# Performance work log

Measured on AMD Instinct MI355X. Metric: run time of the kernel, lower is better.

The kernel has to match this reference:

```python
import jax, jax.numpy as jnp
import numpy as np

D_MODEL = 1024
NUM_EXPERTS = 8


def setup_inputs() -> dict:
    key = jax.random.key(0)
    k_x, k_wg, k_bg, k_we, k_be = jax.random.split(key, 5)
    B, S, D, E = 4, 2048, D_MODEL, NUM_EXPERTS
    x = jax.random.normal(k_x, (B, S, D), dtype=jnp.float32)
    # gate: nn.Linear(d_model, num_experts) -> weight [E, D], bias [E]
    Wg = jax.random.normal(k_wg, (E, D), dtype=jnp.float32) * 0.02
    bg = jax.random.normal(k_bg, (E,), dtype=jnp.float32) * 0.02
    # experts: E x nn.Linear(d_model, d_model) -> weights [E, D, D], biases [E, D]
    We = jax.random.normal(k_we, (E, D, D), dtype=jnp.float32) * 0.02
    be = jax.random.normal(k_be, (E, D), dtype=jnp.float32) * 0.02
    return {"x": x, "Wg": Wg, "bg": bg, "We": We, "be": be, "top_k": 2}


def reference(x, Wg, bg, We, be, top_k):
    # gate_scores: softmax over experts. x:[B,S,D], Wg:[E,D] -> [B,S,E]
    gate_scores = jax.nn.softmax(jnp.einsum("bsd,ed->bse", x, Wg) + bg, axis=-1)
    top_k_values, top_k_indices = jax.lax.top_k(gate_scores, top_k)  # [B,S,K]
    # dense all-expert compute (faithful to original): [B,S,D,E]
    expert_outputs = jnp.einsum("bsd,ekd->bske", x, We) + be.T  # be.T: [D,E]
    # gather top-k experts along last dim: idx broadcast over feature dim D
    top_k_outputs = jnp.take_along_axis(
        expert_outputs, top_k_indices[:, :, None, :], axis=-1
    )  # [B,S,D,K]
    weighted = (top_k_outputs * top_k_values[:, :, None, :]).sum(axis=-1)  # [B,S,D]
    return weighted
```

## Files before the change

### kernel.cpp

```cpp
#include <hip/hip_runtime.h>
#include <hip/hip_bf16.h>
#include <stdint.h>

#define D_MODEL 1024
#define NUM_EXPERTS 8
#define NBUCKET 16
#define BM 128
#define BN 128
#define BK 64
#define KSTEPS (D_MODEL / BK)
#define GATE_TOK 16
#define GATE_BLOCKS 512
#define CONV_BLOCKS 4096
#define GEMM_GRID 2048
#define NWORK 8192

typedef __bf16 bf16x8 __attribute__((ext_vector_type(8)));
typedef float f32x4 __attribute__((ext_vector_type(4)));
typedef unsigned short u16x8 __attribute__((ext_vector_type(8)));

__device__ __forceinline__ unsigned short f32_to_bf16_rne(float f) {
    union { float f; uint32_t u; } v;
    v.f = f;
    uint32_t u = v.u;
    u += 0x7FFFu + ((u >> 16) & 1u);
    return (unsigned short)(u >> 16);
}

__device__ __forceinline__ float bf16_to_f32(unsigned short h) {
    union { uint32_t u; float f; } v;
    v.u = ((uint32_t)h) << 16;
    return v.f;
}

__device__ __forceinline__ void gload_lds16(const unsigned short* g, unsigned short* l) {
    __builtin_amdgcn_global_load_lds(
        (const __attribute__((address_space(1))) void*)g,
        (__attribute__((address_space(3))) void*)l,
        16, 0, 0);
}

__global__ __launch_bounds__(256) void prep_kernel(
    const float* __restrict__ x, const float* __restrict__ Wg,
    const float* __restrict__ bg, const float* __restrict__ We, int T,
    int* __restrict__ counts, int* __restrict__ token_list,
    float* __restrict__ gate_list, unsigned short* __restrict__ xb,
    unsigned short* __restrict__ wbv)
{
    const int tid = threadIdx.x;

    if (blockIdx.x >= GATE_BLOCKS) {
        int g = (blockIdx.x - GATE_BLOCKS) * 256 + tid;
        int s   = g & 7;
        int kt  = (g >> 3) & (KSTEPS - 1);
        int n   = (g >> 7) & 1023;
        int e   = g >> 17;

        const float* sp = We + (size_t)g * 8;
        float4 a = ((const float4*)sp)[0];
        float4 b = ((const float4*)sp)[1];
        u16x8 o;
        o[0] = f32_to_bf16_rne(a.x);
        o[1] = f32_to_bf16_rne(a.y);
        o[2] = f32_to_bf16_rne(a.z);
        o[3] = f32_to_bf16_rne(a.w);
        o[4] = f32_to_bf16_rne(b.x);
        o[5] = f32_to_bf16_rne(b.y);
        o[6] = f32_to_bf16_rne(b.z);
        o[7] = f32_to_bf16_rne(b.w);

        int ss = s ^ (n & 7);
        unsigned short* dp =
            wbv + (((size_t)(e * KSTEPS + kt) * 1024 + n) * BK) + ss * 8;
        *(u16x8*)dp = o;
        return;
    }

    const int lane = tid & 63;
    const int wave = tid >> 6;
    const int tokBase = blockIdx.x * GATE_TOK;

    __shared__ float4 WgS[NUM_EXPERTS * 256];
    __shared__ double logitS[GATE_TOK][NUM_EXPERTS];
    __shared__ int cntS[NBUCKET];
    __shared__ int baseS[NBUCKET];

    if (tid < NBUCKET) cntS[tid] = 0;
#pragma unroll
    for (int i = 0; i < 8; i++)
        WgS[i * 256 + tid] = ((const float4*)Wg)[i * 256 + tid];
    __syncthreads();

    for (int tt = 0; tt < GATE_TOK / 4; tt++) {
        const int lt = wave * (GATE_TOK / 4) + tt;
        const int token = tokBase + lt;
        const float4* xr4 = (const float4*)(x + (size_t)token * D_MODEL);
        ushort4* xbr4 = (ushort4*)(xb + (size_t)token * D_MODEL);

        float4 xv[4];
#pragma unroll
        for (int q = 0; q < 4; q++) {
            float4 f = xr4[q * 64 + lane];
            xv[q] = f;
            ushort4 o;
            o.x = f32_to_bf16_rne(f.x);
            o.y = f32_to_bf16_rne(f.y);
            o.z = f32_to_bf16_rne(f.z);
            o.w = f32_to_bf16_rne(f.w);
            xbr4[q * 64 + lane] = o;
        }

        double acc[NUM_EXPERTS];
#pragma unroll
        for (int e = 0; e < NUM_EXPERTS; e++) {
            double a = 0.0;
#pragma unroll
            for (int q = 0; q < 4; q++) {
                float4 w = WgS[e * 256 + q * 64 + lane];
                a += (double)xv[q].x * (double)w.x;
                a += (double)xv[q].y * (double)w.y;
                a += (double)xv[q].z * (double)w.z;
                a += (double)xv[q].w * (double)w.w;
            }
            acc[e] = a;
        }
#pragma unroll
        for (int e = 0; e < NUM_EXPERTS; e++) {
            double a = acc[e];
            for (int off = 32; off > 0; off >>= 1) a += __shfl_xor(a, off, 64);
            acc[e] = a;
        }
        if (lane == 0) {
#pragma unroll
            for (int e = 0; e < NUM_EXPERTS; e++)
                logitS[lt][e] = acc[e] + (double)bg[e];
        }
    }
    __syncthreads();

    int i1 = 0, i2 = 0, o1 = 0, o2 = 0;
    double v1d = 0.0, v2d = 0.0;
    const int token2 = tokBase + tid;
    if (tid < GATE_TOK) {
        double lg[NUM_EXPERTS];
#pragma unroll
        for (int e = 0; e < NUM_EXPERTS; e++) lg[e] = logitS[tid][e];
        i1 = 0;
#pragma unroll
        for (int e = 1; e < NUM_EXPERTS; e++) if (lg[e] > lg[i1]) i1 = e;
        i2 = (i1 == 0) ? 1 : 0;
#pragma unroll
        for (int e = 0; e < NUM_EXPERTS; e++)
            if (e != i1 && lg[e] > lg[i2]) i2 = e;
        double m = lg[i1], den = 0.0;
#pragma unroll
        for (int e = 0; e < NUM_EXPERTS; e++) den += exp(lg[e] - m);
        v1d = exp(lg[i1] - m) / den;
        v2d = exp(lg[i2] - m) / den;
        o1 = atomicAdd(&cntS[i1], 1);
        o2 = atomicAdd(&cntS[8 + i2], 1);
    }
    __syncthreads();
    if (tid < NBUCKET) baseS[tid] = atomicAdd(&counts[tid], cntS[tid]);
    __syncthreads();
    if (tid < GATE_TOK) {
        int p1 = i1 * T + baseS[i1] + o1;
        token_list[p1] = token2;
        gate_list[p1]  = (float)v1d;
        int p2 = (8 + i2) * T + baseS[8 + i2] + o2;
        token_list[p2] = token2;
        gate_list[p2]  = (float)v2d;
    }
}

__global__ __launch_bounds__(256) void moe_gemm(
    const unsigned short* __restrict__ xb,
    const unsigned short* __restrict__ wb,
    const float* __restrict__ be,
    const int* __restrict__ counts,
    const int* __restrict__ token_list,
    const float* __restrict__ gate_list,
    unsigned short* __restrict__ ybuf,
    int T)
{
    const int tid = threadIdx.x;
    const int wave = tid >> 6, lane = tid & 63;
    const int wm = (wave >> 1) * 64, wn = (wave & 1) * 64;
    const int frow = lane & 15;
    const int qq = lane >> 4;
    const int sw8 = frow & 7;

    __shared__ __align__(16) unsigned short As[2][BM * BK];
    __shared__ __align__(16) unsigned short Bs[2][BN * BK];
    __shared__ int   tokS[BM];
    __shared__ float gateS[BM];

    for (int work = blockIdx.x; work < NWORK; work += GEMM_GRID) {
        const int nt = work & 7;
        const int rest = work >> 3;
        const int vexp = rest & (NBUCKET - 1);
        const int mt = rest >> 4;
        const int e_w = vexp & 7;

        const int n_e = counts[vexp];
        const int m0 = mt * BM;
        if (m0 >= n_e) continue;
        const int n0 = nt * BN;

        __syncthreads();

        if (tid < BM) {
            int r = m0 + tid;
            int tk = 0; float gv = 0.f;
            if (r < n_e) {
                tk = token_list[vexp * T + r];
                gv = gate_list[vexp * T + r];
            }
            tokS[tid]  = tk;
            gateS[tid] = gv;
        }
        __syncthreads();

        const unsigned short* asrc[4];
#pragma unroll
        for (int i = 0; i < 4; i++) {
            int flat = i * 256 + tid;
            int r = flat >> 3, seg = flat & 7;
            int ss = seg ^ (r & 7);
            asrc[i] = xb + (size_t)tokS[r] * D_MODEL + ss * 8;
        }
        const unsigned short* bsrc =
            wb + (size_t)e_w * (KSTEPS * 1024 * BK) + (size_t)n0 * BK;

        f32x4 acc[4][4];
#pragma unroll
        for (int mi = 0; mi < 4; mi++)
#pragma unroll
            for (int ni = 0; ni < 4; ni++)
                acc[mi][ni] = (f32x4){0.f, 0.f, 0.f, 0.f};

#pragma unroll
        for (int i = 0; i < 4; i++) {
            int flat = i * 256 + tid;
            gload_lds16(asrc[i], &As[0][flat * 8]);
            gload_lds16(bsrc + flat * 8, &Bs[0][flat * 8]);
        }
        __syncthreads();

#pragma unroll 2
        for (int kt = 0; kt < KSTEPS; kt++) {
            const int cur = kt & 1;
            if (kt + 1 < KSTEPS) {
#pragma unroll
                for (int i = 0; i < 4; i++) {
                    int flat = i * 256 + tid;
                    gload_lds16(asrc[i] + (kt + 1) * BK, &As[cur ^ 1][flat * 8]);
                    gload_lds16(bsrc + (size_t)(kt + 1) * (1024 * BK) + flat * 8,
                                &Bs[cur ^ 1][flat * 8]);
                }
            }
#pragma unroll
            for (int ks = 0; ks < 2; ks++) {
                const int off = ((ks * 4 + qq) ^ sw8) * 8;
                bf16x8 af[4], bfv[4];
#pragma unroll
                for (int mi = 0; mi < 4; mi++)
                    af[mi] = *(const bf16x8*)&As[cur][(wm + mi * 16 + frow) * BK + off];
#pragma unroll
                for (int ni = 0; ni < 4; ni++)
                    bfv[ni] = *(const bf16x8*)&Bs[cur][(wn + ni * 16 + frow) * BK + off];
#pragma unroll
                for (int mi = 0; mi < 4; mi++)
#pragma unroll
                    for (int ni = 0; ni < 4; ni++)
                        acc[mi][ni] = __builtin_amdgcn_mfma_f32_16x16x32_bf16(
                            af[mi], bfv[ni], acc[mi][ni], 0, 0, 0);
            }
            __syncthreads();
        }

        unsigned short* ybase = ybuf + (size_t)(vexp >> 3) * T * D_MODEL;
        const int rbase = (lane >> 4) * 4;
        const int col   = lane & 15;
#pragma unroll
        for (int mi = 0; mi < 4; mi++) {
#pragma unroll
            for (int r = 0; r < 4; r++) {
                int lrow = wm + mi * 16 + rbase + r;
                if (m0 + lrow < n_e) {
                    int   tk = tokS[lrow];
                    float gv = gateS[lrow];
                    unsigned short* yr = ybase + (size_t)tk * D_MODEL;
#pragma unroll
                    for (int ni = 0; ni < 4; ni++) {
                        int c = n0 + wn + ni * 16 + col;
                        float val = gv * (acc[mi][ni][r] + be[e_w * D_MODEL + c]);
                        yr[c] = f32_to_bf16_rne(val);
                    }
                }
            }
        }
    }
}

__global__ __launch_bounds__(256) void combine_kernel(
    const unsigned short* __restrict__ y0,
    const unsigned short* __restrict__ y1,
    float* __restrict__ out, int n4)
{
    for (int i = blockIdx.x * 256 + threadIdx.x; i < n4; i += 2048 * 256) {
        ushort4 a = ((const ushort4*)y0)[i];
        ushort4 b = ((const ushort4*)y1)[i];
        float4 o;
        o.x = bf16_to_f32(a.x) + bf16_to_f32(b.x);
        o.y = bf16_to_f32(a.y) + bf16_to_f32(b.y);
        o.z = bf16_to_f32(a.z) + bf16_to_f32(b.z);
        o.w = bf16_to_f32(a.w) + bf16_to_f32(b.w);
        ((float4*)out)[i] = o;
    }
}

extern "C" void kernel_launch(void* const* d_in, const int* in_sizes, int n_in,
                              void* d_out, int out_size, void* d_ws, size_t ws_size,
                              hipStream_t stream) {
    const float* x  = (const float*)d_in[0];
    const float* Wg = (const float*)d_in[1];
    const float* bg = (const float*)d_in[2];
    const float* We = (const float*)d_in[3];
    const float* be = (const float*)d_in[4];

    const int T = in_sizes[0] / D_MODEL;

    char* ws = (char*)d_ws;
    unsigned short* xb = (unsigned short*)ws;
    size_t off = (size_t)T * D_MODEL * 2;
    unsigned short* wbv = (unsigned short*)(ws + off);
    off += (size_t)NUM_EXPERTS * D_MODEL * D_MODEL * 2;
    int* counts = (int*)(ws + off);         off += 256;
    int* token_list = (int*)(ws + off);     off += (size_t)NBUCKET * T * 4;
    float* gate_list = (float*)(ws + off);  off += (size_t)NBUCKET * T * 4;
    unsigned short* ybuf = (unsigned short*)(ws + off);
    off += (size_t)2 * T * D_MODEL * 2;

    hipMemsetAsync(counts, 0, 256, stream);

    prep_kernel<<<GATE_BLOCKS + CONV_BLOCKS, 256, 0, stream>>>(
        x, Wg, bg, We, T, counts, token_list, gate_list, xb, wbv);

    moe_gemm<<<GEMM_GRID, 256, 0, stream>>>(
        xb, wbv, be, counts, token_list, gate_list, ybuf, T);

    int n4c = T * D_MODEL / 4;
    combine_kernel<<<2048, 256, 0, stream>>>(
        ybuf, ybuf + (size_t)T * D_MODEL, (float*)d_out, n4c);
}
```

Measured before the change: 222.2 us.

## Fuse gating, weight conversion, grouped GEMM and combine into one cooperative kernel

Merges the prep, GEMM and combine kernels into a single persistent cooperative kernel whose phases are separated by grid-wide syncs, with a grid sized from occupancy and capped at 512 blocks. This removes two kernel launches and their launch gaps. The weight conversion loop is reindexed so consecutive threads read contiguous We rows, and the GEMM main loop swaps __syncthreads for explicit vmcnt waits and raw s_barrier so the next tile's loads stay in flight. In exchange the GEMM runs on far fewer blocks (at most 2 per CU), the kernel depends on cooperative launch, and grid.sync adds its own overhead.

Result: slower. 389.7 us (+75.4%).

```diff
diff --git a/kernel.cpp b/kernel.cpp
--- a/kernel.cpp
+++ b/kernel.cpp
@@ -1,6 +1,9 @@
 #include <hip/hip_runtime.h>
+#include <hip/hip_cooperative_groups.h>
 #include <hip/hip_bf16.h>
 #include <stdint.h>
+
+namespace cg = cooperative_groups;
 
 #define D_MODEL 1024
 #define NUM_EXPERTS 8
@@ -10,10 +13,9 @@
 #define BK 64
 #define KSTEPS (D_MODEL / BK)
 #define GATE_TOK 16
-#define GATE_BLOCKS 512
-#define CONV_BLOCKS 4096
-#define GEMM_GRID 2048
-#define NWORK 8192
+#define GATE_WORKS 512
+#define NSEG (NUM_EXPERTS * KSTEPS * 1024 * 8)
+#define GRID_MAX 512
 
 typedef __bf16 bf16x8 __attribute__((ext_vector_type(8)));
 typedef float f32x4 __attribute__((ext_vector_type(4)));
@@ -40,23 +42,131 @@
         16, 0, 0);
 }
 
-__global__ __launch_bounds__(256) void prep_kernel(
+__global__ __launch_bounds__(256, 2) void fused_moe(
     const float* __restrict__ x, const float* __restrict__ Wg,
-    const float* __restrict__ bg, const float* __restrict__ We, int T,
-    int* __restrict__ counts, int* __restrict__ token_list,
-    float* __restrict__ gate_list, unsigned short* __restrict__ xb,
-    unsigned short* __restrict__ wbv)
+    const float* __restrict__ bg, const float* __restrict__ We,
+    const float* __restrict__ be, int T,
+    int* __restrict__ counts,
+    int* __restrict__ token_list, float* __restrict__ gate_list,
+    unsigned short* __restrict__ xb, unsigned short* __restrict__ wbv,
+    unsigned short* __restrict__ ybuf, float* __restrict__ out)
 {
-    const int tid = threadIdx.x;
-
-    if (blockIdx.x >= GATE_BLOCKS) {
-        int g = (blockIdx.x - GATE_BLOCKS) * 256 + tid;
+    cg::grid_group grid = cg::this_grid();
+
+    const int tid  = threadIdx.x;
+    const int bid  = blockIdx.x;
+    const int lane = tid & 63;
+    const int wave = tid >> 6;
+
+    __shared__ __align__(16) unsigned char smem[66560];
+    float4* WgS = (float4*)smem;
+    double (*logitS)[NUM_EXPERTS] = (double (*)[NUM_EXPERTS])(smem + 32768);
+    int* cntS  = (int*)(smem + 33792);
+    int* baseS = (int*)(smem + 33856);
+    unsigned short* AsB = (unsigned short*)smem;
+    unsigned short* BsB = (unsigned short*)(smem + 32768);
+    int*   tokS  = (int*)(smem + 65536);
+    float* gateS = (float*)(smem + 66048);
+
+#pragma unroll
+    for (int i = 0; i < 8; i++)
+        WgS[i * 256 + tid] = ((const float4*)Wg)[i * 256 + tid];
+
+    for (int w = bid; w < GATE_WORKS; w += gridDim.x) {
+        __syncthreads();
+        if (tid < NBUCKET) cntS[tid] = 0;
+        __syncthreads();
+
+        const int tokBase = w * GATE_TOK;
+        for (int tt = 0; tt < GATE_TOK / 4; tt++) {
+            const int lt = wave * (GATE_TOK / 4) + tt;
+            const int token = tokBase + lt;
+            const float4* xr4 = (const float4*)(x + (size_t)token * D_MODEL);
+            ushort4* xbr4 = (ushort4*)(xb + (size_t)token * D_MODEL);
+
+            float4 xv[4];
+#pragma unroll
+            for (int q = 0; q < 4; q++) {
+                float4 f = xr4[q * 64 + lane];
+                xv[q] = f;
+                ushort4 o;
+                o.x = f32_to_bf16_rne(f.x);
+                o.y = f32_to_bf16_rne(f.y);
+                o.z = f32_to_bf16_rne(f.z);
+                o.w = f32_to_bf16_rne(f.w);
+                xbr4[q * 64 + lane] = o;
+            }
+
+            double acc[NUM_EXPERTS];
+#pragma unroll
+            for (int e = 0; e < NUM_EXPERTS; e++) {
+                double a = 0.0;
+#pragma unroll
+                for (int q = 0; q < 4; q++) {
+                    float4 wv = WgS[e * 256 + q * 64 + lane];
+                    a += (double)xv[q].x * (double)wv.x;
+                    a += (double)xv[q].y * (double)wv.y;
+                    a += (double)xv[q].z * (double)wv.z;
+                    a += (double)xv[q].w * (double)wv.w;
+                }
+                acc[e] = a;
+            }
+#pragma unroll
+            for (int e = 0; e < NUM_EXPERTS; e++) {
+                double a = acc[e];
+                for (int off = 32; off > 0; off >>= 1) a += __shfl_xor(a, off, 64);
+                acc[e] = a;
+            }
+            if (lane == 0) {
+#pragma unroll
+                for (int e = 0; e < NUM_EXPERTS; e++)
+                    logitS[lt][e] = acc[e] + (double)bg[e];
+            }
+        }
+        __syncthreads();
+
+        int i1 = 0, i2 = 0, o1 = 0, o2 = 0;
+        double v1d = 0.0, v2d = 0.0;
+        const int token2 = tokBase + tid;
+        if (tid < GATE_TOK) {
+            double lg[NUM_EXPERTS];
+#pragma unroll
+            for (int e = 0; e < NUM_EXPERTS; e++) lg[e] = logitS[tid][e];
+            i1 = 0;
+#pragma unroll
+            for (int e = 1; e < NUM_EXPERTS; e++) if (lg[e] > lg[i1]) i1 = e;
+            i2 = (i1 == 0) ? 1 : 0;
+#pragma unroll
+            for (int e = 0; e < NUM_EXPERTS; e++)
+                if (e != i1 && lg[e] > lg[i2]) i2 = e;
+            double m = lg[i1], den = 0.0;
+#pragma unroll
+            for (int e = 0; e < NUM_EXPERTS; e++) den += exp(lg[e] - m);
+            v1d = exp(lg[i1] - m) / den;
+            v2d = exp(lg[i2] - m) / den;
+            o1 = atomicAdd(&cntS[i1], 1);
+            o2 = atomicAdd(&cntS[8 + i2], 1);
+        }
+        __syncthreads();
+        if (tid < NBUCKET) baseS[tid] = atomicAdd(&counts[tid], cntS[tid]);
+        __syncthreads();
+        if (tid < GATE_TOK) {
+            int p1 = i1 * T + baseS[i1] + o1;
+            token_list[p1] = token2;
+            gate_list[p1]  = (float)v1d;
+            int p2 = (8 + i2) * T + baseS[8 + i2] + o2;
+            token_list[p2] = token2;
+            gate_list[p2]  = (float)v2d;
+        }
+    }
+
+    for (int g = bid * 256 + tid; g < NSEG; g += gridDim.x * 256) {
         int s   = g & 7;
-        int kt  = (g >> 3) & (KSTEPS - 1);
-        int n   = (g >> 7) & 1023;
+        int n   = (g >> 3) & 1023;
+        int kt  = (g >> 13) & (KSTEPS - 1);
         int e   = g >> 17;
 
-        const float* sp = We + (size_t)g * 8;
+        const float* sp = We + ((size_t)(e * 1024 + n)) * 1024 + kt * BK + s * 8;
         float4 a = ((const float4*)sp)[0];
         float4 b = ((const float4*)sp)[1];
         u16x8 o;
@@ -73,129 +183,14 @@
         unsigned short* dp =
             wbv + (((size_t)(e * KSTEPS + kt) * 1024 + n) * BK) + ss * 8;
         *(u16x8*)dp = o;
-        return;
-    }
-
-    const int lane = tid & 63;
-    const int wave = tid >> 6;
-    const int tokBase = blockIdx.x * GATE_TOK;
-
-    __shared__ float4 WgS[NUM_EXPERTS * 256];
-    __shared__ double logitS[GATE_TOK][NUM_EXPERTS];
-    __shared__ int cntS[NBUCKET];
-    __shared__ int baseS[NBUCKET];
-
-    if (tid < NBUCKET) cntS[tid] = 0;
-#pragma unroll
-    for (int i = 0; i < 8; i++)
-        WgS[i * 256 + tid] = ((const float4*)Wg)[i * 256 + tid];
-    __syncthreads();
-
-    for (int tt = 0; tt < GATE_TOK / 4; tt++) {
-        const int lt = wave * (GATE_TOK / 4) + tt;
-        const int token = tokBase + lt;
-        const float4* xr4 = (const float4*)(x + (size_t)token * D_MODEL);
-        ushort4* xbr4 = (ushort4*)(xb + (size_t)token * D_MODEL);
-
-        float4 xv[4];
-#pragma unroll
-        for (int q = 0; q < 4; q++) {
-            float4 f = xr4[q * 64 + lane];
-            xv[q] = f;
-            ushort4 o;
-            o.x = f32_to_bf16_rne(f.x);
-            o.y = f32_to_bf16_rne(f.y);
-            o.z = f32_to_bf16_rne(f.z);
-            o.w = f32_to_bf16_rne(f.w);
-            xbr4[q * 64 + lane] = o;
-        }
-
-        double acc[NUM_EXPERTS];
-#pragma unroll
-        for (int e = 0; e < NUM_EXPERTS; e++) {
-            double a = 0.0;
-#pragma unroll
-            for (int q = 0; q < 4; q++) {
-                float4 w = WgS[e * 256 + q * 64 + lane];
-                a += (double)xv[q].x * (double)w.x;
-                a += (double)xv[q].y * (double)w.y;
-                a += (double)xv[q].z * (double)w.z;
-                a += (double)xv[q].w * (double)w.w;
-            }
-            acc[e] = a;
-        }
-#pragma unroll
-        for (int e = 0; e < NUM_EXPERTS; e++) {
-            double a = acc[e];
-            for (int off = 32; off > 0; off >>= 1) a += __shfl_xor(a, off, 64);
-            acc[e] = a;
-        }
-        if (lane == 0) {
-#pragma unroll
-            for (int e = 0; e < NUM_EXPERTS; e++)
-                logitS[lt][e] = acc[e] + (double)bg[e];
-        }
-    }
-    __syncthreads();
-
-    int i1 = 0, i2 = 0, o1 = 0, o2 = 0;
-    double v1d = 0.0, v2d = 0.0;
-    const int token2 = tokBase + tid;
-    if (tid < GATE_TOK) {
-        double lg[NUM_EXPERTS];
-#pragma unroll
-        for (int e = 0; e < NUM_EXPERTS; e++) lg[e] = logitS[tid][e];
-        i1 = 0;
-#pragma unroll
-        for (int e = 1; e < NUM_EXPERTS; e++) if (lg[e] > lg[i1]) i1 = e;
-        i2 = (i1 == 0) ? 1 : 0;
-#pragma unroll
-        for (int e = 0; e < NUM_EXPERTS; e++)
-            if (e != i1 && lg[e] > lg[i2]) i2 = e;
-        double m = lg[i1], den = 0.0;
-#pragma unroll
-        for (int e = 0; e < NUM_EXPERTS; e++) den += exp(lg[e] - m);
-        v1d = exp(lg[i1] - m) / den;
-        v2d = exp(lg[i2] - m) / den;
-        o1 = atomicAdd(&cntS[i1], 1);
-        o2 = atomicAdd(&cntS[8 + i2], 1);
-    }
-    __syncthreads();
-    if (tid < NBUCKET) baseS[tid] = atomicAdd(&counts[tid], cntS[tid]);
-    __syncthreads();
-    if (tid < GATE_TOK) {
-        int p1 = i1 * T + baseS[i1] + o1;
-        token_list[p1] = token2;
-        gate_list[p1]  = (float)v1d;
-        int p2 = (8 + i2) * T + baseS[8 + i2] + o2;
-        token_list[p2] = token2;
-        gate_list[p2]  = (float)v2d;
-    }
-}
-
-__global__ __launch_bounds__(256) void moe_gemm(
-    const unsigned short* __restrict__ xb,
-    const unsigned short* __restrict__ wb,
-    const float* __restrict__ be,
-    const int* __restrict__ counts,
-    const int* __restrict__ token_list,
-    const float* __restrict__ gate_list,
-    unsigned short* __restrict__ ybuf,
-    int T)
-{
-    const int tid = threadIdx.x;
-    const int wave = tid >> 6, lane = tid & 63;
-    const int wm = (wave >> 1) * 64, wn = (wave & 1) * 64;
-    const int frow = lane & 15;
-    const int qq = lane >> 4;
-    const int sw8 = frow & 7;
-
-    __shared__ __align__(16) unsigned short As[2][BM * BK];
-    __shared__ __align__(16) unsigned short Bs[2][BN * BK];
-    __shared__ int   tokS[BM];
-    __shared__ float gateS[BM];
-
-    for (int work = blockIdx.x; work < NWORK; work += GEMM_GRID) {
+    }
+
+    __threadfence();
+    grid.sync();
+    __threadfence();
+
+    const int nWork = ((T + BM - 1) / BM) * NBUCKET * 8;
+    for (int work = bid; work < nWork; work += gridDim.x) {
         const int nt = work & 7;
         const int rest = work >> 3;
         const int vexp = rest & (NBUCKET - 1);
@@ -230,7 +225,12 @@
             asrc[i] = xb + (size_t)tokS[r] * D_MODEL + ss * 8;
         }
         const unsigned short* bsrc =
-            wb + (size_t)e_w * (KSTEPS * 1024 * BK) + (size_t)n0 * BK;
+            wbv + (size_t)e_w * (KSTEPS * 1024 * BK) + (size_t)n0 * BK;
+
+        const int wm = (wave >> 1) * 64, wn = (wave & 1) * 64;
+        const int frow = lane & 15;
+        const int qq = lane >> 4;
+        const int sw8 = frow & 7;
 
         f32x4 acc[4][4];
 #pragma unroll
@@ -242,33 +242,43 @@
 #pragma unroll
         for (int i = 0; i < 4; i++) {
             int flat = i * 256 + tid;
-            gload_lds16(asrc[i], &As[0][flat * 8]);
-            gload_lds16(bsrc + flat * 8, &Bs[0][flat * 8]);
-        }
-        __syncthreads();
+            gload_lds16(asrc[i], AsB + flat * 8);
+            gload_lds16(bsrc + flat * 8, BsB + flat * 8);
+        }
 
 #pragma unroll 2
         for (int kt = 0; kt < KSTEPS; kt++) {
             const int cur = kt & 1;
+            unsigned short* Ac = AsB + cur * (BM * BK);
+            unsigned short* Bc = BsB + cur * (BN * BK);
             if (kt + 1 < KSTEPS) {
+                unsigned short* An = AsB + (cur ^ 1) * (BM * BK);
+                unsigned short* Bn = BsB + (cur ^ 1) * (BN * BK);
 #pragma unroll
                 for (int i = 0; i < 4; i++) {
                     int flat = i * 256 + tid;
-                    gload_lds16(asrc[i] + (kt + 1) * BK, &As[cur ^ 1][flat * 8]);
+                    gload_lds16(asrc[i] + (kt + 1) * BK, An + flat * 8);
                     gload_lds16(bsrc + (size_t)(kt + 1) * (1024 * BK) + flat * 8,
-                                &Bs[cur ^ 1][flat * 8]);
+                                Bn + flat * 8);
                 }
-            }
+                asm volatile("s_waitcnt vmcnt(8)" ::: "memory");
+            } else {
+                asm volatile("s_waitcnt vmcnt(0)" ::: "memory");
+            }
+            __builtin_amdgcn_sched_barrier(0);
+            __builtin_amdgcn_s_barrier();
+            __builtin_amdgcn_sched_barrier(0);
+
 #pragma unroll
             for (int ks = 0; ks < 2; ks++) {
                 const int off = ((ks * 4 + qq) ^ sw8) * 8;
                 bf16x8 af[4], bfv[4];
 #pragma unroll
                 for (int mi = 0; mi < 4; mi++)
-                    af[mi] = *(const bf16x8*)&As[cur][(wm + mi * 16 + frow) * BK + off];
+                    af[mi] = *(const bf16x8*)&Ac[(wm + mi * 16 + frow) * BK + off];
 #pragma unroll
                 for (int ni = 0; ni < 4; ni++)
-                    bfv[ni] = *(const bf16x8*)&Bs[cur][(wn + ni * 16 + frow) * BK + off];
+                    bfv[ni] = *(const bf16x8*)&Bc[(wn + ni * 16 + frow) * BK + off];
 #pragma unroll
                 for (int mi = 0; mi < 4; mi++)
 #pragma unroll
@@ -276,7 +286,9 @@
                         acc[mi][ni] = __builtin_amdgcn_mfma_f32_16x16x32_bf16(
                             af[mi], bfv[ni], acc[mi][ni], 0, 0, 0);
             }
-            __syncthreads();
+            __builtin_amdgcn_sched_barrier(0);
+            __builtin_amdgcn_s_barrier();
+            __builtin_amdgcn_sched_barrier(0);
         }
 
         unsigned short* ybase = ybuf + (size_t)(vexp >> 3) * T * D_MODEL;
@@ -301,14 +313,15 @@
             }
         }
     }
-}
-
-__global__ __launch_bounds__(256) void combine_kernel(
-    const unsigned short* __restrict__ y0,
-    const unsigned short* __restrict__ y1,
-    float* __restrict__ out, int n4)
-{
-    for (int i = blockIdx.x * 256 + threadIdx.x; i < n4; i += 2048 * 256) {
+
+    __threadfence();
+    grid.sync();
+    __threadfence();
+
+    const unsigned short* y0 = ybuf;
+    const unsigned short* y1 = ybuf + (size_t)T * D_MODEL;
+    const int n4c = T * D_MODEL / 4;
+    for (int i = bid * 256 + tid; i < n4c; i += gridDim.x * 256) {
         ushort4 a = ((const ushort4*)y0)[i];
         ushort4 b = ((const ushort4*)y1)[i];
         float4 o;
@@ -329,7 +342,7 @@
     const float* We = (const float*)d_in[3];
     const float* be = (const float*)d_in[4];
 
-    const int T = in_sizes[0] / D_MODEL;
+    int T = in_sizes[0] / D_MODEL;
 
     char* ws = (char*)d_ws;
     unsigned short* xb = (unsigned short*)ws;
@@ -341,16 +354,25 @@
     float* gate_list = (float*)(ws + off);  off += (size_t)NBUCKET * T * 4;
     unsigned short* ybuf = (unsigned short*)(ws + off);
     off += (size_t)2 * T * D_MODEL * 2;
+    float* outp = (float*)d_out;
+
+    static int s_grid = 0;
+    if (s_grid == 0) {
+        int nb = 0;
+        if (hipOccupancyMaxActiveBlocksPerMultiprocessor(&nb, fused_moe, 256, 0)
+                != hipSuccess || nb < 1)
+            nb = 1;
+        int g = nb * 256;
+        s_grid = g < GRID_MAX ? g : GRID_MAX;
+    }
 
     hipMemsetAsync(counts, 0, 256, stream);
 
-    prep_kernel<<<GATE_BLOCKS + CONV_BLOCKS, 256, 0, stream>>>(
-        x, Wg, bg, We, T, counts, token_list, gate_list, xb, wbv);
-
-    moe_gemm<<<GEMM_GRID, 256, 0, stream>>>(
-        xb, wbv, be, counts, token_list, gate_list, ybuf, T);
-
-    int n4c = T * D_MODEL / 4;
-    combine_kernel<<<2048, 256, 0, stream>>>(
-        ybuf, ybuf + (size_t)T * D_MODEL, (float*)d_out, n4c);
-}
+    void* kargs[] = {
+        (void*)&x, (void*)&Wg, (void*)&bg, (void*)&We, (void*)&be, (void*)&T,
+        (void*)&counts, (void*)&token_list, (void*)&gate_list,
+        (void*)&xb, (void*)&wbv, (void*)&ybuf, (void*)&outp
+    };
+    hipLaunchCooperativeKernel((const void*)fused_moe, dim3(s_grid), dim3(256),
+                               kargs, 0, stream);
+}
```
